# Performance work log

Measured on AMD Instinct MI355X. Metric: run time of the kernel, lower is better.

## Reference

```python
import jax, jax.numpy as jnp
import numpy as np

N = 512
D = 512
# static upper-triangle pair indices (i < j)
_II, _JJ = np.triu_indices(N, k=1)
_II = jnp.asarray(_II)
_JJ = jnp.asarray(_JJ)


def setup_inputs() -> dict:
    key = jax.random.key(0)
    ks = jax.random.split(key, 9)
    s = 0.02
    return {
        'features': jax.random.normal(ks[0], (N, D), dtype=jnp.float32),
        # relation_classifier: Linear(2D->D), Linear(D->10)
        'cw1': jax.random.normal(ks[1], (2 * D, D), dtype=jnp.float32) * s,
        'cb1': jnp.zeros((D,), dtype=jnp.float32),
        'cw2': jax.random.normal(ks[2], (D, 10), dtype=jnp.float32) * s,
        'cb2': jnp.zeros((10,), dtype=jnp.float32),
        # relation_strength_calc: Linear(2D->D//2), Linear(D//2->1)
        'sw1': jax.random.normal(ks[3], (2 * D, D // 2), dtype=jnp.float32) * s,
        'sb1': jnp.zeros((D // 2,), dtype=jnp.float32),
        'sw2': jax.random.normal(ks[4], (D // 2, 1), dtype=jnp.float32) * s,
        'sb2': jnp.zeros((1,), dtype=jnp.float32),
    }


def reference(features, cw1, cb1, cw2, cb2, sw1, sb1, sw2, sb2):
    # cat([f_i, f_j]) @ W == f_i @ W[:D] + f_j @ W[D:]  (linear-split trick)
    # precompute per-node projections once, then gather per pair
    c_a = features @ cw1[:D]   # [N, D]
    c_b = features @ cw1[D:]   # [N, D]
    s_a = features @ sw1[:D]   # [N, D//2]
    s_b = features @ sw1[D:]   # [N, D//2]

    # classifier path
    h = jax.nn.relu(c_a[_II] + c_b[_JJ] + cb1)          # [P, D]
    relation_types = jax.nn.log_softmax(h @ cw2 + cb2)   # [P, 10]
    most_likely_relations = jnp.argmax(relation_types, axis=-1)  # [P]

    # strength path
    hs = jax.nn.relu(s_a[_II] + s_b[_JJ] + sb1)          # [P, D//2]
    relation_strengths = jax.nn.sigmoid(hs @ sw2 + sb2)   # [P, 1]

    return relation_types, most_likely_relations, relation_strengths
```

## Files before the change

kernel.cpp:

```cpp
#include <hip/hip_runtime.h>
#include <math.h>

#define NN 512
#define DD 512
#define NPAIRS 130816
#define TYPES_OFF 0
#define ARGMAX_OFF 1308160
#define STRENGTH_OFF 1438976

#define GAP_THRESH 2.5e-4f


__device__ __forceinline__ void fma64_step4(
    const float4& a0, const float4& a1, const float4& a2, const float4& a3,
    const float4& b0, const float4& b1, const float4& b2, const float4& b3,
    double acc[4][4])
{
    const float av[4][4] = {{a0.x,a0.y,a0.z,a0.w},{a1.x,a1.y,a1.z,a1.w},
                            {a2.x,a2.y,a2.z,a2.w},{a3.x,a3.y,a3.z,a3.w}};
    const float bv[4][4] = {{b0.x,b0.y,b0.z,b0.w},{b1.x,b1.y,b1.z,b1.w},
                            {b2.x,b2.y,b2.z,b2.w},{b3.x,b3.y,b3.z,b3.w}};
    #pragma unroll
    for (int kk = 0; kk < 4; ++kk) {
        double bd0 = (double)bv[kk][0], bd1 = (double)bv[kk][1];
        double bd2 = (double)bv[kk][2], bd3 = (double)bv[kk][3];
        #pragma unroll
        for (int rr = 0; rr < 4; ++rr) {
            double ad = (double)av[rr][kk];
            acc[rr][0] = fma(ad, bd0, acc[rr][0]);
            acc[rr][1] = fma(ad, bd1, acc[rr][1]);
            acc[rr][2] = fma(ad, bd2, acc[rr][2]);
            acc[rr][3] = fma(ad, bd3, acc[rr][3]);
        }
    }
}

__device__ __forceinline__ void fma32_step4(
    const float4& a0, const float4& a1, const float4& a2, const float4& a3,
    const float4& b0, const float4& b1, const float4& b2, const float4& b3,
    float acc[4][4])
{
    const float av[4][4] = {{a0.x,a0.y,a0.z,a0.w},{a1.x,a1.y,a1.z,a1.w},
                            {a2.x,a2.y,a2.z,a2.w},{a3.x,a3.y,a3.z,a3.w}};
    const float bv[4][4] = {{b0.x,b0.y,b0.z,b0.w},{b1.x,b1.y,b1.z,b1.w},
                            {b2.x,b2.y,b2.z,b2.w},{b3.x,b3.y,b3.z,b3.w}};
    #pragma unroll
    for (int kk = 0; kk < 4; ++kk) {
        #pragma unroll
        for (int rr = 0; rr < 4; ++rr) {
            #pragma unroll
            for (int cc = 0; cc < 4; ++cc)
                acc[rr][cc] = fmaf(av[rr][kk], bv[kk][cc], acc[rr][cc]);
        }
    }
}

__global__ __launch_bounds__(256, 2) void proj_kernel(
    const float* __restrict__ F, const float* __restrict__ cw1,
    const float* __restrict__ sw1,
    const float* __restrict__ cb1, const float* __restrict__ sb1,
    double* __restrict__ ca0, double* __restrict__ ca1,
    double* __restrict__ ca2, double* __restrict__ ca3,
    double* __restrict__ cb0, double* __restrict__ cb1p,
    double* __restrict__ cb2p, double* __restrict__ cb3p,
    float* __restrict__ sa0, float* __restrict__ sa1,
    float* __restrict__ sb0, float* __restrict__ sbp1)
{
    const int t = threadIdx.x;
    const int w = t >> 6;
    const int lane = t & 63;
    const int mg = lane >> 4;
    const int nq = lane & 15;

    if (blockIdx.x < 512) {
        const int b  = blockIdx.x;
        const int z  = b & 3;
        const int nt = (b >> 2) & 15;
        const int mt = b >> 6;
        const int n  = nt * 64;
        const float* W = (n < 512) ? cw1 : cw1 + 512 * 512;
        const int n0   = (n < 512) ? n : n - 512;
        double* outp;
        if (n < 512) outp = (z == 0) ? ca0 : (z == 1) ? ca1 : (z == 2) ? ca2 : ca3;
        else         outp = (z == 0) ? cb0 : (z == 1) ? cb1p : (z == 2) ? cb2p : cb3p;
        const bool addbias = (z == 0) && (n < 512);

        const int row0 = mt * 64 + w * 16 + mg * 4;
        const int col0 = n0 + nq * 4;
        const float* pa = F + row0 * 512 + z * 128;
        const float* pb = W + (z * 128) * 512 + col0;

        double acc[4][4];
        #pragma unroll
        for (int rr = 0; rr < 4; ++rr)
            #pragma unroll
            for (int cc = 0; cc < 4; ++cc) acc[rr][cc] = 0.0;

        float4 a0 = *(const float4*)(pa);
        float4 a1 = *(const float4*)(pa + 512);
        float4 a2 = *(const float4*)(pa + 1024);
        float4 a3 = *(const float4*)(pa + 1536);
        float4 b0 = *(const float4*)(pb);
        float4 b1 = *(const float4*)(pb + 512);
        float4 b2 = *(const float4*)(pb + 1024);
        float4 b3 = *(const float4*)(pb + 1536);
        for (int s = 0; s < 31; ++s) {
            const float* npa = pa + (s + 1) * 4;
            float4 na0 = *(const float4*)(npa);
            float4 na1 = *(const float4*)(npa + 512);
            float4 na2 = *(const float4*)(npa + 1024);
            float4 na3 = *(const float4*)(npa + 1536);
            const float* nb = pb + (s + 1) * 2048;
            float4 nb0 = *(const float4*)(nb);
            float4 nb1 = *(const float4*)(nb + 512);
            float4 nb2 = *(const float4*)(nb + 1024);
            float4 nb3 = *(const float4*)(nb + 1536);
            fma64_step4(a0, a1, a2, a3, b0, b1, b2, b3, acc);
            a0 = na0; a1 = na1; a2 = na2; a3 = na3;
            b0 = nb0; b1 = nb1; b2 = nb2; b3 = nb3;
        }
        fma64_step4(a0, a1, a2, a3, b0, b1, b2, b3, acc);

        #pragma unroll
        for (int rr = 0; rr < 4; ++rr) {
            double v[4];
            #pragma unroll
            for (int cc = 0; cc < 4; ++cc) {
                v[cc] = acc[rr][cc];
                if (addbias) v[cc] += (double)cb1[col0 + cc];
            }
            double* dst = outp + (row0 + rr) * 512 + col0;
            *(double2*)(dst + 0) = make_double2(v[0], v[1]);
            *(double2*)(dst + 2) = make_double2(v[2], v[3]);
        }
    } else {
        const int sbk = blockIdx.x - 512;
        const int z  = sbk & 1;
        const int nt = (sbk >> 1) & 7;
        const int mt = sbk >> 4;
        const int n  = nt * 64;
        const float* W = (n < 256) ? sw1 : sw1 + 512 * 256;
        const int n0   = (n < 256) ? n : n - 256;
        float* outp    = (n < 256) ? (z ? sa1 : sa0) : (z ? sbp1 : sb0);
        const bool addbias = (z == 0) && (n < 256);

        const int row0 = mt * 64 + w * 16 + mg * 4;
        const int col0 = n0 + nq * 4;
        const float* pa = F + row0 * 512 + z * 256;
        const float* pb = W + (z * 256) * 256 + col0;

        float acc[4][4];
        #pragma unroll
        for (int rr = 0; rr < 4; ++rr)
            #pragma unroll
            for (int cc = 0; cc < 4; ++cc) acc[rr][cc] = 0.f;

        float4 a0 = *(const float4*)(pa);
        float4 a1 = *(const float4*)(pa + 512);
        float4 a2 = *(const float4*)(pa + 1024);
        float4 a3 = *(const float4*)(pa + 1536);
        float4 b0 = *(const float4*)(pb);
        float4 b1 = *(const float4*)(pb + 256);
        float4 b2 = *(const float4*)(pb + 512);
        float4 b3 = *(const float4*)(pb + 768);
        for (int s = 0; s < 63; ++s) {
            const float* npa = pa + (s + 1) * 4;
            float4 na0 = *(const float4*)(npa);
            float4 na1 = *(const float4*)(npa + 512);
            float4 na2 = *(const float4*)(npa + 1024);
            float4 na3 = *(const float4*)(npa + 1536);
            const float* nb = pb + (s + 1) * 1024;
            float4 nb0 = *(const float4*)(nb);
            float4 nb1 = *(const float4*)(nb + 256);
            float4 nb2 = *(const float4*)(nb + 512);
            float4 nb3 = *(const float4*)(nb + 768);
            fma32_step4(a0, a1, a2, a3, b0, b1, b2, b3, acc);
            a0 = na0; a1 = na1; a2 = na2; a3 = na3;
            b0 = nb0; b1 = nb1; b2 = nb2; b3 = nb3;
        }
        fma32_step4(a0, a1, a2, a3, b0, b1, b2, b3, acc);

        #pragma unroll
        for (int rr = 0; rr < 4; ++rr) {
            float4 v = make_float4(acc[rr][0], acc[rr][1], acc[rr][2], acc[rr][3]);
            if (addbias) {
                v.x += sb1[col0 + 0]; v.y += sb1[col0 + 1];
                v.z += sb1[col0 + 2]; v.w += sb1[col0 + 3];
            }
            *(float4*)(outp + (row0 + rr) * 256 + col0) = v;
        }
    }
}

__global__ __launch_bounds__(256) void combine_kernel(
    const double* __restrict__ ca0, const double* __restrict__ ca1,
    const double* __restrict__ ca2, const double* __restrict__ ca3,
    const double* __restrict__ cb0, const double* __restrict__ cb1p,
    const double* __restrict__ cb2p, const double* __restrict__ cb3p,
    const float* __restrict__ sa0, const float* __restrict__ sa1,
    const float* __restrict__ sb0, const float* __restrict__ sbp1,
    float* __restrict__ cfa, float* __restrict__ cfb,
    float* __restrict__ sfa, float* __restrict__ sfb)
{
    const int t = blockIdx.x * 256 + threadIdx.x;
    {
        const int e = 2 * t;
        double2 x0 = *(const double2*)(ca0 + e);
        double2 x1 = *(const double2*)(ca1 + e);
        double2 x2 = *(const double2*)(ca2 + e);
        double2 x3 = *(const double2*)(ca3 + e);
        *(float2*)(cfa + e) = make_float2(
            (float)((x0.x + x1.x) + (x2.x + x3.x)),
            (float)((x0.y + x1.y) + (x2.y + x3.y)));
        double2 y0 = *(const double2*)(cb0 + e);
        double2 y1 = *(const double2*)(cb1p + e);
        double2 y2 = *(const double2*)(cb2p + e);
        double2 y3 = *(const double2*)(cb3p + e);
        *(float2*)(cfb + e) = make_float2(
            (float)((y0.x + y1.x) + (y2.x + y3.x)),
            (float)((y0.y + y1.y) + (y2.y + y3.y)));
    }
    if (t < 65536) {
        const bool second = t >= 32768;
        const int e = (second ? (t - 32768) : t) * 4;
        const float* s0 = second ? sb0 : sa0;
        const float* s1 = second ? sbp1 : sa1;
        float* dst      = second ? sfb : sfa;
        float4 a = *(const float4*)(s0 + e);
        float4 b = *(const float4*)(s1 + e);
        *(float4*)(dst + e) = make_float4(a.x + b.x, a.y + b.y, a.z + b.z, a.w + b.w);
    }
}

__global__ __launch_bounds__(256, 4) void pair_kernel(
    const double* __restrict__ ca0, const double* __restrict__ ca1,
    const double* __restrict__ ca2, const double* __restrict__ ca3,
    const double* __restrict__ cb0, const double* __restrict__ cb1p,
    const double* __restrict__ cb2p, const double* __restrict__ cb3p,
    const float* __restrict__ cfa, const float* __restrict__ cfb,
    const float* __restrict__ sfa, const float* __restrict__ sfb,
    const float* __restrict__ cw2, const float* __restrict__ cb2,
    const float* __restrict__ sw2, const float* __restrict__ sb2,
    float* __restrict__ out)
{
    const int b = blockIdx.x;
    int bi = (int)floorf((129.0f - sqrtf(16641.0f - 8.0f * (float)b)) * 0.5f);
    while ((bi + 1) * (129 - (bi + 1)) / 2 <= b) ++bi;
    while (bi * (129 - bi) / 2 > b) --bi;
    const int bj = bi + (b - bi * (129 - bi) / 2);
    const int i0 = bi * 8, j0 = bj * 8;

    const int t = threadIdx.x;
    const int q  = t >> 6;
    const int qu = __builtin_amdgcn_readfirstlane(q);
    const int l = t & 63;
    const int pi = l >> 3, pj = l & 7;
    const int i = i0 + pi, j = j0 + pj;

    __shared__ __align__(16) float smem[4352];
    float* sSa = smem;
    float* sSb = smem + 2176;
    float* sA  = smem;
    float* sB  = smem + 2176;
    float* lgbuf = smem;
    float* stbuf = smem + 1920;

    #pragma unroll
    for (int u = 0; u < 4; ++u) {
        int idx = u * 256 + t;
        int kq  = idx & 15;
        int row = (idx >> 4) & 7;
        int qq  = (idx >> 7) & 3;
        int arr = idx >> 9;
        int off = (arr ? (j0 + row) : (i0 + row)) * 256 + qq * 64 + kq * 4;
        const float* src = arr ? sfb : sfa;
        float4 v = *(const float4*)(src + off);
        float* dst = (arr ? sSb : sSa) + (qq * 8 + row) * 68 + kq * 4;
        *(float4*)dst = v;
    }
    __syncthreads();
    float accs = 0.f;
    {
        const float* sw2q = sw2 + qu * 64;
        const float* ra = sSa + (q * 8 + pi) * 68;
        const float* rb = sSb + (q * 8 + pj) * 68;
        float p0 = 0.f, p1 = 0.f, p2 = 0.f, p3 = 0.f;
        for (int kk = 0; kk < 64; kk += 4) {
            float4 a4 = *(const float4*)(ra + kk);
            float4 b4 = *(const float4*)(rb + kk);
            p0 = fmaf(fmaxf(a4.x + b4.x, 0.f), sw2q[kk + 0], p0);
            p1 = fmaf(fmaxf(a4.y + b4.y, 0.f), sw2q[kk + 1], p1);
            p2 = fmaf(fmaxf(a4.z + b4.z, 0.f), sw2q[kk + 2], p2);
            p3 = fmaf(fmaxf(a4.w + b4.w, 0.f), sw2q[kk + 3], p3);
        }
        accs = (p0 + p1) + (p2 + p3);
    }

    float lg[10];
    #pragma unroll
    for (int c = 0; c < 10; ++c) lg[c] = 0.f;

    for (int rnd = 0; rnd < 2; ++rnd) {
        __syncthreads();
        #pragma unroll
        for (int u = 0; u < 4; ++u) {
            int idx = u * 256 + t;
            int kq  = idx & 15;
            int row = (idx >> 4) & 7;
            int qq  = (idx >> 7) & 3;
            int arr = idx >> 9;
            int off = (arr ? (j0 + row) : (i0 + row)) * 512 + qq * 128 + rnd * 64 + kq * 4;
            const float* src = arr ? cfb : cfa;
            float4 v = *(const float4*)(src + off);
            float* dst = (arr ? sB : sA) + (qq * 8 + row) * 68 + kq * 4;
            *(float4*)dst = v;
        }
        __syncthreads();
        const float* ra = sA + (q * 8 + pi) * 68;
        const float* rb = sB + (q * 8 + pj) * 68;
        const float* wr = cw2 + (qu * 128 + rnd * 64) * 10;
        for (int kk = 0; kk < 64; kk += 4) {
            float4 ra4 = *(const float4*)(ra + kk);
            float4 rb4 = *(const float4*)(rb + kk);
            float h0 = fmaxf(ra4.x + rb4.x, 0.f);
            float h1 = fmaxf(ra4.y + rb4.y, 0.f);
            float h2 = fmaxf(ra4.z + rb4.z, 0.f);
            float h3 = fmaxf(ra4.w + rb4.w, 0.f);
            const float* w = wr + kk * 10;
            #pragma unroll
            for (int c = 0; c < 10; ++c) lg[c] = fmaf(h0, w[c], lg[c]);
            #pragma unroll
            for (int c = 0; c < 10; ++c) lg[c] = fmaf(h1, w[10 + c], lg[c]);
            #pragma unroll
            for (int c = 0; c < 10; ++c) lg[c] = fmaf(h2, w[20 + c], lg[c]);
            #pragma unroll
            for (int c = 0; c < 10; ++c) lg[c] = fmaf(h3, w[30 + c], lg[c]);
        }
    }

    __syncthreads();
    if (q > 0) {
        float* dst = lgbuf + ((q - 1) * 64 + l) * 10;
        #pragma unroll
        for (int c = 0; c < 10; ++c) dst[c] = lg[c];
        stbuf[(q - 1) * 64 + l] = accs;
    }
    __syncthreads();
    if (q == 0) {
        #pragma unroll
        for (int w = 0; w < 3; ++w) {
            const float* srcb = lgbuf + (w * 64 + l) * 10;
            #pragma unroll
            for (int c = 0; c < 10; ++c) lg[c] += srcb[c];
        }
        float st = accs + stbuf[l] + stbuf[64 + l] + stbuf[128 + l] + sb2[0];

        #pragma unroll
        for (int c = 0; c < 10; ++c) lg[c] += cb2[c];

        float mx = lg[0], mx2 = -3.0e38f; int am2 = 0;
        #pragma unroll
        for (int c = 1; c < 10; ++c) {
            if (lg[c] > mx) { mx2 = mx; mx = lg[c]; am2 = c; }
            else if (lg[c] > mx2) mx2 = lg[c];
        }

        unsigned long long m = __ballot((j > i) && (mx - mx2 < GAP_THRESH));
        while (m) {
            const int s = __ffsll((unsigned long long)m) - 1; m &= (m - 1);
            const int si = i0 + (s >> 3), sj = j0 + (s & 7);
            double part[10];
            #pragma unroll
            for (int c = 0; c < 10; ++c) part[c] = 0.0;
            const int kb = l * 8;
            #pragma unroll 2
            for (int kk = 0; kk < 8; ++kk) {
                const int k = kb + kk;
                const int ei = si * 512 + k, ej = sj * 512 + k;
                double va = (ca0[ei] + ca1[ei]) + (ca2[ei] + ca3[ei]);
                double vb = (cb0[ej] + cb1p[ej]) + (cb2p[ej] + cb3p[ej]);
                double h = fmax(va + vb, 0.0);
                const float* w = cw2 + k * 10;
                #pragma unroll
                for (int c = 0; c < 10; ++c) part[c] = fma(h, (double)w[c], part[c]);
            }
            #pragma unroll
            for (int off = 32; off > 0; off >>= 1) {
                #pragma unroll
                for (int c = 0; c < 10; ++c) part[c] += __shfl_xor(part[c], off, 64);
            }
            double bmx = part[0] + (double)cb2[0]; int ba = 0;
            #pragma unroll
            for (int c = 1; c < 10; ++c) {
                double v = part[c] + (double)cb2[c];
                if (v > bmx) { bmx = v; ba = c; }
            }
            if (l == s) am2 = ba;
        }

        float tf[10]; float ssum = 0.f;
        #pragma unroll
        for (int c = 0; c < 10; ++c) { tf[c] = lg[c] - mx; ssum += __expf(tf[c]); }
        float ls = __logf(ssum);

        if (j > i) {
            const int p = i * 511 - (i * (i - 1)) / 2 + (j - i - 1);
            float* tp = out + TYPES_OFF + p * 10;
            #pragma unroll
            for (int c = 0; c < 10; ++c) tp[c] = tf[c] - ls;
            out[ARGMAX_OFF + p] = (float)am2;
            out[STRENGTH_OFF + p] = 1.0f / (1.0f + __expf(-st));
        }
    }
}

extern "C" void kernel_launch(void* const* d_in, const int* in_sizes, int n_in,
                              void* d_out, int out_size, void* d_ws, size_t ws_size,
                              hipStream_t stream) {
    const float* F   = (const float*)d_in[0];
    const float* cw1 = (const float*)d_in[1];
    const float* cb1 = (const float*)d_in[2];
    const float* cw2 = (const float*)d_in[3];
    const float* cb2 = (const float*)d_in[4];
    const float* sw1 = (const float*)d_in[5];
    const float* sb1 = (const float*)d_in[6];
    const float* sw2 = (const float*)d_in[7];
    const float* sb2 = (const float*)d_in[8];
    float* out = (float*)d_out;

    char* ws = (char*)d_ws;
    double* ca0  = (double*)(ws);
    double* ca1  = (double*)(ws + 2097152);
    double* ca2  = (double*)(ws + 4194304);
    double* ca3  = (double*)(ws + 6291456);
    double* cb0  = (double*)(ws + 8388608);
    double* cb1p = (double*)(ws + 10485760);
    double* cb2p = (double*)(ws + 12582912);
    double* cb3p = (double*)(ws + 14680064);
    float*  sa0  = (float*)(ws + 16777216);
    float*  sa1  = (float*)(ws + 17301504);
    float*  sb0  = (float*)(ws + 17825792);
    float*  sbp1 = (float*)(ws + 18350080);
    float*  cfa  = (float*)(ws + 18874368);
    float*  cfb  = (float*)(ws + 19922944);
    float*  sfa  = (float*)(ws + 20971520);
    float*  sfb  = (float*)(ws + 21495808);

    hipLaunchKernelGGL(proj_kernel, dim3(640), dim3(256), 0, stream,
                       F, cw1, sw1, cb1, sb1,
                       ca0, ca1, ca2, ca3, cb0, cb1p, cb2p, cb3p,
                       sa0, sa1, sb0, sbp1);
    hipLaunchKernelGGL(combine_kernel, dim3(512), dim3(256), 0, stream,
                       ca0, ca1, ca2, ca3, cb0, cb1p, cb2p, cb3p,
                       sa0, sa1, sb0, sbp1, cfa, cfb, sfa, sfb);
    hipLaunchKernelGGL(pair_kernel, dim3(2080), dim3(256), 0, stream,
                       ca0, ca1, ca2, ca3, cb0, cb1p, cb2p, cb3p,
                       cfa, cfb, sfa, sfb, cw2, cb2, sw2, sb2, out);
}
```

Baseline: 144.9 us.

## Use 16x16 pair tiles with full-K per thread in pair kernel

The pair kernel now uses 16x16 node tiles instead of 8x8, with each of the four waves owning an 8x8 sub-tile and reducing over the full hidden dimension itself. This replaces the previous split-K across waves and its shared-memory reduction. Each block loads the full projection rows into LDS once (about 66KB), which cuts the number of blocks from 2080 to 528 and halves the global row reads per pair. In exchange, occupancy drops (launch bounds 2, large LDS), there are fewer blocks to fill the CUs, and each thread runs a longer serial FMA chain.

```diff
diff --git a/kernel.cpp b/kernel.cpp
--- a/kernel.cpp
+++ b/kernel.cpp
@@ -232,7 +232,7 @@
     }
 }
 
-__global__ __launch_bounds__(256, 4) void pair_kernel(
+__global__ __launch_bounds__(256, 2) void pair_kernel(
     const double* __restrict__ ca0, const double* __restrict__ ca1,
     const double* __restrict__ ca2, const double* __restrict__ ca3,
     const double* __restrict__ cb0, const double* __restrict__ cb1p,
@@ -244,89 +244,86 @@
     float* __restrict__ out)
 {
     const int b = blockIdx.x;
-    int bi = (int)floorf((129.0f - sqrtf(16641.0f - 8.0f * (float)b)) * 0.5f);
-    while ((bi + 1) * (129 - (bi + 1)) / 2 <= b) ++bi;
-    while (bi * (129 - bi) / 2 > b) --bi;
-    const int bj = bi + (b - bi * (129 - bi) / 2);
-    const int i0 = bi * 8, j0 = bj * 8;
+    int bi = (int)floorf((65.0f - sqrtf(4225.0f - 8.0f * (float)b)) * 0.5f);
+    while ((bi + 1) * (65 - (bi + 1)) / 2 <= b) ++bi;
+    while (bi * (65 - bi) / 2 > b) --bi;
+    const int bj = bi + (b - bi * (65 - bi) / 2);
+    const int i0 = bi * 16, j0 = bj * 16;
 
     const int t = threadIdx.x;
-    const int q  = t >> 6;
-    const int qu = __builtin_amdgcn_readfirstlane(q);
+    const int q = t >> 6;
     const int l = t & 63;
-    const int pi = l >> 3, pj = l & 7;
+    const int wr = (q >> 1) * 8;
+    const int wc = (q & 1) * 8;
+    const int pi = wr + (l >> 3), pj = wc + (l & 7);
     const int i = i0 + pi, j = j0 + pj;
 
-    __shared__ __align__(16) float smem[4352];
+    __shared__ __align__(16) float smem[16512];
+    float* sA  = smem;
+    float* sB  = smem + 8256;
     float* sSa = smem;
-    float* sSb = smem + 2176;
-    float* sA  = smem;
-    float* sB  = smem + 2176;
-    float* lgbuf = smem;
-    float* stbuf = smem + 1920;
-
-    #pragma unroll
-    for (int u = 0; u < 4; ++u) {
+    float* sSb = smem + 4160;
+
+    #pragma unroll
+    for (int u = 0; u < 8; ++u) {
         int idx = u * 256 + t;
-        int kq  = idx & 15;
-        int row = (idx >> 4) & 7;
-        int qq  = (idx >> 7) & 3;
-        int arr = idx >> 9;
-        int off = (arr ? (j0 + row) : (i0 + row)) * 256 + qq * 64 + kq * 4;
+        int arr = idx >> 10;
+        int e   = idx & 1023;
+        int row = e >> 6;
+        int c4  = e & 63;
         const float* src = arr ? sfb : sfa;
-        float4 v = *(const float4*)(src + off);
-        float* dst = (arr ? sSb : sSa) + (qq * 8 + row) * 68 + kq * 4;
+        int gr = (arr ? j0 : i0) + row;
+        float4 v = *(const float4*)(src + gr * 256 + c4 * 4);
+        float* dst = (arr ? sSb : sSa) + row * 260 + c4 * 4;
         *(float4*)dst = v;
     }
     __syncthreads();
-    float accs = 0.f;
+    float accs;
     {
-        const float* sw2q = sw2 + qu * 64;
-        const float* ra = sSa + (q * 8 + pi) * 68;
-        const float* rb = sSb + (q * 8 + pj) * 68;
+        const float* ra = sSa + pi * 260;
+        const float* rb = sSb + pj * 260;
         float p0 = 0.f, p1 = 0.f, p2 = 0.f, p3 = 0.f;
-        for (int kk = 0; kk < 64; kk += 4) {
+        for (int kk = 0; kk < 256; kk += 4) {
             float4 a4 = *(const float4*)(ra + kk);
             float4 b4 = *(const float4*)(rb + kk);
-            p0 = fmaf(fmaxf(a4.x + b4.x, 0.f), sw2q[kk + 0], p0);
-            p1 = fmaf(fmaxf(a4.y + b4.y, 0.f), sw2q[kk + 1], p1);
-            p2 = fmaf(fmaxf(a4.z + b4.z, 0.f), sw2q[kk + 2], p2);
-            p3 = fmaf(fmaxf(a4.w + b4.w, 0.f), sw2q[kk + 3], p3);
+            p0 = fmaf(fmaxf(a4.x + b4.x, 0.f), sw2[kk + 0], p0);
+            p1 = fmaf(fmaxf(a4.y + b4.y, 0.f), sw2[kk + 1], p1);
+            p2 = fmaf(fmaxf(a4.z + b4.z, 0.f), sw2[kk + 2], p2);
+            p3 = fmaf(fmaxf(a4.w + b4.w, 0.f), sw2[kk + 3], p3);
         }
         accs = (p0 + p1) + (p2 + p3);
     }
+    __syncthreads();
+
+    #pragma unroll
+    for (int u = 0; u < 16; ++u) {
+        int idx = u * 256 + t;
+        int arr = idx >> 11;
+        int e   = idx & 2047;
+        int row = e >> 7;
+        int c4  = e & 127;
+        const float* src = arr ? cfb : cfa;
+        int gr = (arr ? j0 : i0) + row;
+        float4 v = *(const float4*)(src + gr * 512 + c4 * 4);
+        float* dst = (arr ? sB : sA) + row * 516 + c4 * 4;
+        *(float4*)dst = v;
+    }
+    __syncthreads();
 
     float lg[10];
     #pragma unroll
     for (int c = 0; c < 10; ++c) lg[c] = 0.f;
-
-    for (int rnd = 0; rnd < 2; ++rnd) {
-        __syncthreads();
-        #pragma unroll
-        for (int u = 0; u < 4; ++u) {
-            int idx = u * 256 + t;
-            int kq  = idx & 15;
-            int row = (idx >> 4) & 7;
-            int qq  = (idx >> 7) & 3;
-            int arr = idx >> 9;
-            int off = (arr ? (j0 + row) : (i0 + row)) * 512 + qq * 128 + rnd * 64 + kq * 4;
-            const float* src = arr ? cfb : cfa;
-            float4 v = *(const float4*)(src + off);
-            float* dst = (arr ? sB : sA) + (qq * 8 + row) * 68 + kq * 4;
-            *(float4*)dst = v;
-        }
-        __syncthreads();
-        const float* ra = sA + (q * 8 + pi) * 68;
-        const float* rb = sB + (q * 8 + pj) * 68;
-        const float* wr = cw2 + (qu * 128 + rnd * 64) * 10;
-        for (int kk = 0; kk < 64; kk += 4) {
+    {
+        const float* ra = sA + pi * 516;
+        const float* rb = sB + pj * 516;
+        for (int kk = 0; kk < 512; kk += 4) {
             float4 ra4 = *(const float4*)(ra + kk);
             float4 rb4 = *(const float4*)(rb + kk);
             float h0 = fmaxf(ra4.x + rb4.x, 0.f);
             float h1 = fmaxf(ra4.y + rb4.y, 0.f);
             float h2 = fmaxf(ra4.z + rb4.z, 0.f);
             float h3 = fmaxf(ra4.w + rb4.w, 0.f);
-            const float* w = wr + kk * 10;
+            const float* w = cw2 + kk * 10;
             #pragma unroll
             for (int c = 0; c < 10; ++c) lg[c] = fmaf(h0, w[c], lg[c]);
             #pragma unroll
@@ -338,79 +335,61 @@
         }
     }
 
-    __syncthreads();
-    if (q > 0) {
-        float* dst = lgbuf + ((q - 1) * 64 + l) * 10;
-        #pragma unroll
-        for (int c = 0; c < 10; ++c) dst[c] = lg[c];
-        stbuf[(q - 1) * 64 + l] = accs;
-    }
-    __syncthreads();
-    if (q == 0) {
-        #pragma unroll
-        for (int w = 0; w < 3; ++w) {
-            const float* srcb = lgbuf + (w * 64 + l) * 10;
-            #pragma unroll
-            for (int c = 0; c < 10; ++c) lg[c] += srcb[c];
-        }
-        float st = accs + stbuf[l] + stbuf[64 + l] + stbuf[128 + l] + sb2[0];
-
-        #pragma unroll
-        for (int c = 0; c < 10; ++c) lg[c] += cb2[c];
-
-        float mx = lg[0], mx2 = -3.0e38f; int am2 = 0;
+    #pragma unroll
+    for (int c = 0; c < 10; ++c) lg[c] += cb2[c];
+
+    float mx = lg[0], mx2 = -3.0e38f; int am2 = 0;
+    #pragma unroll
+    for (int c = 1; c < 10; ++c) {
+        if (lg[c] > mx) { mx2 = mx; mx = lg[c]; am2 = c; }
+        else if (lg[c] > mx2) mx2 = lg[c];
+    }
+
+    unsigned long long m = __ballot((j > i) && (mx - mx2 < GAP_THRESH));
+    while (m) {
+        const int s = __ffsll((unsigned long long)m) - 1; m &= (m - 1);
+        const int si = i0 + wr + (s >> 3), sj = j0 + wc + (s & 7);
+        double part[10];
+        #pragma unroll
+        for (int c = 0; c < 10; ++c) part[c] = 0.0;
+        const int kb = l * 8;
+        #pragma unroll 2
+        for (int kk = 0; kk < 8; ++kk) {
+            const int k = kb + kk;
+            const int ei = si * 512 + k, ej = sj * 512 + k;
+            double va = (ca0[ei] + ca1[ei]) + (ca2[ei] + ca3[ei]);
+            double vb = (cb0[ej] + cb1p[ej]) + (cb2p[ej] + cb3p[ej]);
+            double h = fmax(va + vb, 0.0);
+            const float* w = cw2 + k * 10;
+            #pragma unroll
+            for (int c = 0; c < 10; ++c) part[c] = fma(h, (double)w[c], part[c]);
+        }
+        #pragma unroll
+        for (int off = 32; off > 0; off >>= 1) {
+            #pragma unroll
+            for (int c = 0; c < 10; ++c) part[c] += __shfl_xor(part[c], off, 64);
+        }
+        double bmx = part[0] + (double)cb2[0]; int ba = 0;
         #pragma unroll
         for (int c = 1; c < 10; ++c) {
-            if (lg[c] > mx) { mx2 = mx; mx = lg[c]; am2 = c; }
-            else if (lg[c] > mx2) mx2 = lg[c];
-        }
-
-        unsigned long long m = __ballot((j > i) && (mx - mx2 < GAP_THRESH));
-        while (m) {
-            const int s = __ffsll((unsigned long long)m) - 1; m &= (m - 1);
-            const int si = i0 + (s >> 3), sj = j0 + (s & 7);
-            double part[10];
-            #pragma unroll
-            for (int c = 0; c < 10; ++c) part[c] = 0.0;
-            const int kb = l * 8;
-            #pragma unroll 2
-            for (int kk = 0; kk < 8; ++kk) {
-                const int k = kb + kk;
-                const int ei = si * 512 + k, ej = sj * 512 + k;
-                double va = (ca0[ei] + ca1[ei]) + (ca2[ei] + ca3[ei]);
-                double vb = (cb0[ej] + cb1p[ej]) + (cb2p[ej] + cb3p[ej]);
-                double h = fmax(va + vb, 0.0);
-                const float* w = cw2 + k * 10;
-                #pragma unroll
-                for (int c = 0; c < 10; ++c) part[c] = fma(h, (double)w[c], part[c]);
-            }
-            #pragma unroll
-            for (int off = 32; off > 0; off >>= 1) {
-                #pragma unroll
-                for (int c = 0; c < 10; ++c) part[c] += __shfl_xor(part[c], off, 64);
-            }
-            double bmx = part[0] + (double)cb2[0]; int ba = 0;
-            #pragma unroll
-            for (int c = 1; c < 10; ++c) {
-                double v = part[c] + (double)cb2[c];
-                if (v > bmx) { bmx = v; ba = c; }
-            }
-            if (l == s) am2 = ba;
-        }
-
-        float tf[10]; float ssum = 0.f;
-        #pragma unroll
-        for (int c = 0; c < 10; ++c) { tf[c] = lg[c] - mx; ssum += __expf(tf[c]); }
-        float ls = __logf(ssum);
-
-        if (j > i) {
-            const int p = i * 511 - (i * (i - 1)) / 2 + (j - i - 1);
-            float* tp = out + TYPES_OFF + p * 10;
-            #pragma unroll
-            for (int c = 0; c < 10; ++c) tp[c] = tf[c] - ls;
-            out[ARGMAX_OFF + p] = (float)am2;
-            out[STRENGTH_OFF + p] = 1.0f / (1.0f + __expf(-st));
-        }
+            double v = part[c] + (double)cb2[c];
+            if (v > bmx) { bmx = v; ba = c; }
+        }
+        if (l == s) am2 = ba;
+    }
+
+    float tf[10]; float ssum = 0.f;
+    #pragma unroll
+    for (int c = 0; c < 10; ++c) { tf[c] = lg[c] - mx; ssum += __expf(tf[c]); }
+    float ls = __logf(ssum);
+
+    if (j > i) {
+        const int p = i * 511 - (i * (i - 1)) / 2 + (j - i - 1);
+        float* tp = out + TYPES_OFF + p * 10;
+        #pragma unroll
+        for (int c = 0; c < 10; ++c) tp[c] = tf[c] - ls;
+        out[ARGMAX_OFF + p] = (float)am2;
+        out[STRENGTH_OFF + p] = 1.0f / (1.0f + __expf(-(accs + sb2[0])));
     }
 }
 
@@ -453,7 +432,7 @@
     hipLaunchKernelGGL(combine_kernel, dim3(512), dim3(256), 0, stream,
                        ca0, ca1, ca2, ca3, cb0, cb1p, cb2p, cb3p,
                        sa0, sa1, sb0, sbp1, cfa, cfb, sfa, sfb);
-    hipLaunchKernelGGL(pair_kernel, dim3(2080), dim3(256), 0, stream,
+    hipLaunchKernelGGL(pair_kernel, dim3(528), dim3(256), 0, stream,
                        ca0, ca1, ca2, ca3, cb0, cb1p, cb2p, cb3p,
                        cfa, cfb, sfa, sfb, cw2, cb2, sw2, sb2, out);
 }
```

New measurement: 191.5 us. 1.32x slower.
